# Optimization experiments

Measured on AMD Instinct MI355X. Metric: run time of the kernel, lower is better.

Reference implementation:

```python
import jax, jax.numpy as jnp
import numpy as np

B, L, H, E = 8, 1024, 8, 64  # self-attention: S=L, D=E
SCALE = 1.0 / np.sqrt(E).astype(np.float32)


def setup_inputs() -> dict:
    key = jax.random.key(0)
    ks = jax.random.split(key, 6)
    shp = (B, L, H, E)
    names = ["q_re", "q_im", "k_re", "k_im", "v_re", "v_im"]
    return {n: jax.random.normal(k, shp, dtype=jnp.float32) for n, k in zip(names, ks)}


def reference(q_re, q_im, k_re, k_im, v_re, v_im):
    q = jax.lax.complex(q_re, q_im)  # [B,L,H,E] complex64
    k = jax.lax.complex(k_re, k_im)  # [B,S,H,E] complex64
    # complex QK^T (no conjugate, matching torch einsum semantics)
    scores = jnp.einsum('blhe,bshe->bhls', q, k)      # [B,H,L,S] complex64
    A = jax.nn.softmax(SCALE * jnp.abs(scores), axis=-1)  # [B,H,L,S] real
    # A is promoted to complex with zero imaginary part in the original;
    # multiplying complex V by a real A is equivalent per real/imag part.
    V_re = jnp.einsum('bhls,bshd->blhd', A, v_re)     # [B,L,H,D]
    V_im = jnp.einsum('bhls,bshd->blhd', A, v_im)     # [B,L,H,D]
    return jnp.stack([V_re, V_im], axis=-1)           # [B,L,H,D,2] (re, im)
```

## Files before the change

### kernel.cpp

```cpp
#include <hip/hip_runtime.h>


#define B_ 8
#define L_ 1024
#define H_ 8
#define E_ 64
#define SB 64
#define QB 128
#define NT 16
#define IMG_BYTES 32768
#define WS_NEEDED (64ull * NT * IMG_BYTES)
#define C_EXP 0.18033688011112042f

typedef float  f32x4  __attribute__((ext_vector_type(4)));
typedef float  f32x16 __attribute__((ext_vector_type(16)));
typedef __bf16 bf16x8 __attribute__((ext_vector_type(8)));
typedef unsigned short u16x8 __attribute__((ext_vector_type(8)));
typedef unsigned short u16x4 __attribute__((ext_vector_type(4)));
typedef unsigned int   u32x4 __attribute__((ext_vector_type(4)));

static __device__ __forceinline__ unsigned short f2b(float f) {
    __bf16 h = (__bf16)f;
    return __builtin_bit_cast(unsigned short, h);
}

static __device__ __forceinline__ float fsqrt_(float x) {
    return __builtin_amdgcn_sqrtf(x);
}
static __device__ __forceinline__ float fexp2_(float x) {
    return __builtin_amdgcn_exp2f(x);
}

static __device__ __forceinline__ u16x8 pack8(float4 a, float4 b) {
    u16x8 t;
    t[0]=f2b(a.x); t[1]=f2b(a.y); t[2]=f2b(a.z); t[3]=f2b(a.w);
    t[4]=f2b(b.x); t[5]=f2b(b.y); t[6]=f2b(b.z); t[7]=f2b(b.w);
    return t;
}

static __device__ __forceinline__ f32x16 mfma32(u16x8 a, u16x8 b, f32x16 c) {
    return __builtin_amdgcn_mfma_f32_32x32x16_bf16(
        __builtin_bit_cast(bf16x8, a), __builtin_bit_cast(bf16x8, b), c, 0, 0, 0);
}

static __device__ __forceinline__ unsigned int cvtpk(float lo, float hi) {
    unsigned int r;
    asm("v_cvt_pk_bf16_f32 %0, %1, %2" : "=v"(r) : "v"(lo), "v"(hi));
    return r;
}

static __device__ __forceinline__ void plswap(unsigned int& x, unsigned int& y) {
    asm("v_permlane32_swap_b32 %0, %1" : "+v"(x), "+v"(y));
}

static __device__ __forceinline__ void gload16(const void* g, void* l) {
    __builtin_amdgcn_global_load_lds(
        (const __attribute__((address_space(1))) void*)g,
        (__attribute__((address_space(3))) void*)l,
        16, 0, 0);
}

__global__ __launch_bounds__(256) void ffa_prepack(
    const float* __restrict__ k_re, const float* __restrict__ k_im,
    const float* __restrict__ v_re, const float* __restrict__ v_im,
    char* __restrict__ ws)
{
    const int tid = threadIdx.x;
    const int bh  = blockIdx.x >> 4;
    const int st  = blockIdx.x & 15;
    const int b   = bh >> 3;
    const int h   = bh & 7;
    const int s0  = st * SB;
    char* const img = ws + (size_t)blockIdx.x * IMG_BYTES;

    {
        const int sr = tid >> 2;
        const int sc = (tid & 3) * 16;
        const int kg = ((b * L_ + s0 + sr) * H_ + h) * E_ + sc;
        const float4* pr = (const float4*)(k_re + kg);
        const float4* pi = (const float4*)(k_im + kg);
        float4 r0 = pr[0], r1 = pr[1], r2 = pr[2], r3 = pr[3];
        float4 i0 = pi[0], i1 = pi[1], i2 = pi[2], i3 = pi[3];
        const int krow = sr * 256;
        const int ksw  = (sr & 7) << 4;
        *(u16x8*)(img + ((krow + sc * 2           ) ^ ksw)) = pack8(r0, r1);
        *(u16x8*)(img + ((krow + sc * 2 + 16      ) ^ ksw)) = pack8(r2, r3);
        *(u16x8*)(img + ((krow + 128 + sc * 2     ) ^ ksw)) = pack8(i0, i1);
        *(u16x8*)(img + ((krow + 128 + sc * 2 + 16) ^ ksw)) = pack8(i2, i3);
    }

    {
        const int vtens = tid >> 7;
        const int vd    = ((tid >> 4) & 7) * 8;
        const int vs    = (tid & 15) * 4;
        const float* const vsrc = vtens ? v_im : v_re;
        float vv[4][8];
#pragma unroll
        for (int j = 0; j < 4; ++j) {
            const float4* p = (const float4*)(vsrc + ((b * L_ + s0 + vs + j) * H_ + h) * E_ + vd);
            float4 x = p[0], y = p[1];
            vv[j][0]=x.x; vv[j][1]=x.y; vv[j][2]=x.z; vv[j][3]=x.w;
            vv[j][4]=y.x; vv[j][5]=y.y; vv[j][6]=y.z; vv[j][7]=y.w;
        }
        char* const vimg = img + 16384;
#pragma unroll
        for (int i = 0; i < 8; ++i) {
            const int row = vtens * 64 + vd + i;
            u16x4 t;
            t[0]=f2b(vv[0][i]); t[1]=f2b(vv[1][i]); t[2]=f2b(vv[2][i]); t[3]=f2b(vv[3][i]);
            *(u16x4*)(vimg + ((row * 128 + vs * 2) ^ ((row & 7) << 4))) = t;
        }
    }
}

__global__ __launch_bounds__(256) void ffa_main(
    const float* __restrict__ q_re, const float* __restrict__ q_im,
    const char* __restrict__ ws, float* __restrict__ out)
{
    __shared__ __align__(16) char Buf[2][IMG_BYTES];

    const int tid  = threadIdx.x;
    const int lane = tid & 63;
    const int w    = tid >> 6;
    const int l31  = lane & 31;
    const int h    = lane >> 5;

    const int work = (blockIdx.x & 7) * 64 + (blockIdx.x >> 3);
    const int bh   = work >> 3;
    const int qblk = work & 7;
    const int b    = bh >> 3;
    const int hh   = bh & 7;
    const char* const imgs = ws + (size_t)bh * (NT * IMG_BYTES);

#pragma unroll
    for (int i = 0; i < 8; ++i)
        gload16(imgs + i * 4096 + tid * 16, Buf[0] + i * 4096 + tid * 16);

    u16x8 qre[4], qim[4], qimn[4];
    {
        const int qrow = qblk * QB + w * 32 + l31;
        const int base = ((b * L_ + qrow) * H_ + hh) * E_;
#pragma unroll
        for (int ks = 0; ks < 4; ++ks) {
            const float4* pr = (const float4*)(q_re + base + ks * 16 + h * 8);
            const float4* pi = (const float4*)(q_im + base + ks * 16 + h * 8);
            qre[ks] = pack8(pr[0], pr[1]);
            qim[ks] = pack8(pi[0], pi[1]);
#pragma unroll
            for (int i = 0; i < 8; ++i)
                qimn[ks][i] = (unsigned short)(qim[ks][i] ^ 0x8000u);
        }
    }

    f32x16 oR0 = {}, oR1 = {}, oI0 = {}, oI1 = {};
    float lsum = 0.f;
    const f32x16 z16 = {};
    const int hsw = (h << 4) ^ ((l31 & 7) << 4);

    asm volatile("s_waitcnt vmcnt(0)" ::: "memory");
    __syncthreads();

    for (int st = 0; st < NT; ++st) {
        const int cur = st & 1;
        if (st + 1 < NT) {
            const char* src = imgs + (size_t)(st + 1) * IMG_BYTES;
            char* dst = Buf[cur ^ 1];
#pragma unroll
            for (int i = 0; i < 8; ++i)
                gload16(src + i * 4096 + tid * 16, dst + i * 4096 + tid * 16);
        }
        const char* const kb = Buf[cur];
        const char* const vb = kb + 16384;

        u16x8 pa[4];

#pragma unroll
        for (int kh = 0; kh < 2; ++kh) {
            const char* krow = kb + kh * 8192 + l31 * 256;
            u16x8 kreF[4], kimF[4];
#pragma unroll
            for (int ks = 0; ks < 4; ++ks) {
                kreF[ks] = *(const u16x8*)(krow + ((      ks * 32) ^ hsw));
                kimF[ks] = *(const u16x8*)(krow + ((128 + ks * 32) ^ hsw));
            }
            __builtin_amdgcn_s_setprio(1);
            f32x16 sR = mfma32(kreF[0], qre[0], z16);
            f32x16 sI = mfma32(kimF[0], qre[0], z16);
            sR = mfma32(kimF[0], qimn[0], sR);
            sI = mfma32(kreF[0], qim[0],  sI);
#pragma unroll
            for (int ks = 1; ks < 4; ++ks) {
                sR = mfma32(kreF[ks], qre[ks],  sR);
                sI = mfma32(kimF[ks], qre[ks],  sI);
                sR = mfma32(kimF[ks], qimn[ks], sR);
                sI = mfma32(kreF[ks], qim[ks],  sI);
            }
            __builtin_amdgcn_s_setprio(0);

            float p[16];
#pragma unroll
            for (int r = 0; r < 16; ++r) {
                float re = sR[r], im = sI[r];
                float mag = fsqrt_(fmaf(re, re, im * im));
                p[r] = fexp2_(mag * C_EXP);
            }
            lsum += (((p[0]+p[1])+(p[2]+p[3])) + ((p[4]+p[5])+(p[6]+p[7])))
                  + (((p[8]+p[9])+(p[10]+p[11])) + ((p[12]+p[13])+(p[14]+p[15])));

            unsigned int a0 = cvtpk(p[0],  p[1]),  a1 = cvtpk(p[4],  p[5]);
            unsigned int a2 = cvtpk(p[2],  p[3]),  a3 = cvtpk(p[6],  p[7]);
            unsigned int b0 = cvtpk(p[8],  p[9]),  b1 = cvtpk(p[12], p[13]);
            unsigned int b2 = cvtpk(p[10], p[11]), b3 = cvtpk(p[14], p[15]);
            plswap(a0, a1);
            plswap(a2, a3);
            plswap(b0, b1);
            plswap(b2, b3);
            u32x4 wa = {a0, a2, a1, a3};
            u32x4 wb = {b0, b2, b1, b3};
            pa[2 * kh]     = __builtin_bit_cast(u16x8, wa);
            pa[2 * kh + 1] = __builtin_bit_cast(u16x8, wb);
        }

        {
            const char* vrow = vb + l31 * 128;
            __builtin_amdgcn_s_setprio(1);
#pragma unroll
            for (int ks = 0; ks < 4; ++ks) {
                const int off = (ks * 32) ^ hsw;
                u16x8 vre0 = *(const u16x8*)(vrow +         off);
                u16x8 vre1 = *(const u16x8*)(vrow +  4096 + off);
                u16x8 vim0 = *(const u16x8*)(vrow +  8192 + off);
                u16x8 vim1 = *(const u16x8*)(vrow + 12288 + off);
                oR0 = mfma32(pa[ks], vre0, oR0);
                oR1 = mfma32(pa[ks], vre1, oR1);
                oI0 = mfma32(pa[ks], vim0, oI0);
                oI1 = mfma32(pa[ks], vim1, oI1);
            }
            __builtin_amdgcn_s_setprio(0);
        }

        asm volatile("s_waitcnt vmcnt(0)" ::: "memory");
        __syncthreads();
    }

    lsum += __shfl_xor(lsum, 32);
    const float inv = 1.0f / lsum;
#pragma unroll
    for (int r = 0; r < 16; ++r) {
        const int qs = (r & 3) + 8 * (r >> 2) + 4 * h;
        const float iv = __shfl(inv, qs);
        const int lq = qblk * QB + w * 32 + qs;
        float* op = out + ((b * L_ + lq) * H_ + hh) * (E_ * 2);
        float2 v0 = make_float2(oR0[r] * iv, oI0[r] * iv);
        float2 v1 = make_float2(oR1[r] * iv, oI1[r] * iv);
        *(float2*)(op + l31 * 2)      = v0;
        *(float2*)(op + 64 + l31 * 2) = v1;
    }
}

__global__ __launch_bounds__(256) void ffa_fwd_fb(
    const float* __restrict__ q_re, const float* __restrict__ q_im,
    const float* __restrict__ k_re, const float* __restrict__ k_im,
    const float* __restrict__ v_re, const float* __restrict__ v_im,
    float* __restrict__ out)
{
    __shared__ __align__(16) unsigned short Kt[64 * 128];
    __shared__ __align__(16) unsigned short Vt[128 * 64];
    __shared__ __align__(16) unsigned short Pw[4 * 16 * 64];
    char* const kb = (char*)Kt;
    char* const vb = (char*)Vt;

    const int tid  = threadIdx.x;
    const int lane = tid & 63;
    const int w    = tid >> 6;
    const int lr   = lane & 15;
    const int lg   = lane >> 4;
    const int lg16 = lg * 16;
    const int qblk = blockIdx.x & 15;
    const int bh   = blockIdx.x >> 4;
    const int b    = bh >> 3;
    const int h    = bh & 7;

    u16x8 qre[2], qim[2], qimn[2];
    {
        const int qrow = qblk * 64 + w * 16 + lr;
        const int base = ((b * L_ + qrow) * H_ + h) * E_ + lg * 8;
#pragma unroll
        for (int ks = 0; ks < 2; ++ks) {
            const float4* pr = (const float4*)(q_re + base + ks * 32);
            const float4* pi = (const float4*)(q_im + base + ks * 32);
            qre[ks] = pack8(pr[0], pr[1]);
            qim[ks] = pack8(pi[0], pi[1]);
#pragma unroll
            for (int i = 0; i < 8; ++i)
                qimn[ks][i] = (unsigned short)(qim[ks][i] ^ 0x8000u);
        }
    }

    float lsum[4];
    f32x4 Ore[4], Oim[4];
    const f32x4 zero = {0.f, 0.f, 0.f, 0.f};
#pragma unroll
    for (int r = 0; r < 4; ++r) lsum[r] = 0.f;
#pragma unroll
    for (int dt = 0; dt < 4; ++dt) { Ore[dt] = zero; Oim[dt] = zero; }

    const int sr = tid >> 2;
    const int sc = (tid & 3) * 16;
    const int vtens = tid >> 7;
    const int vd    = ((tid >> 4) & 7) * 8;
    const int vs    = (tid & 15) * 4;
    const float* const vsrc = vtens ? v_im : v_re;

    for (int st = 0; st < L_ / SB; ++st) {
        const int s0 = st * SB;
        {
            const int kg = ((b * L_ + s0 + sr) * H_ + h) * E_ + sc;
            const float4* pr = (const float4*)(k_re + kg);
            const float4* pi = (const float4*)(k_im + kg);
            float4 r0 = pr[0], r1 = pr[1], r2 = pr[2], r3 = pr[3];
            float4 i0 = pi[0], i1 = pi[1], i2 = pi[2], i3 = pi[3];
            const int krow = sr * 256;
            const int ksw  = (sr & 7) << 4;
            *(u16x8*)(kb + ((krow + sc * 2           ) ^ ksw)) = pack8(r0, r1);
            *(u16x8*)(kb + ((krow + sc * 2 + 16      ) ^ ksw)) = pack8(r2, r3);
            *(u16x8*)(kb + ((krow + 128 + sc * 2     ) ^ ksw)) = pack8(i0, i1);
            *(u16x8*)(kb + ((krow + 128 + sc * 2 + 16) ^ ksw)) = pack8(i2, i3);
        }
        {
            float vv[4][8];
#pragma unroll
            for (int j = 0; j < 4; ++j) {
                const float4* p = (const float4*)(vsrc + ((b * L_ + s0 + vs + j) * H_ + h) * E_ + vd);
                float4 x = p[0], y = p[1];
                vv[j][0]=x.x; vv[j][1]=x.y; vv[j][2]=x.z; vv[j][3]=x.w;
                vv[j][4]=y.x; vv[j][5]=y.y; vv[j][6]=y.z; vv[j][7]=y.w;
            }
#pragma unroll
            for (int i = 0; i < 8; ++i) {
                const int row = vtens * 64 + vd + i;
                u16x4 t;
                t[0]=f2b(vv[0][i]); t[1]=f2b(vv[1][i]); t[2]=f2b(vv[2][i]); t[3]=f2b(vv[3][i]);
                *(u16x4*)(vb + ((row * 128 + vs * 2) ^ ((row & 7) << 4))) = t;
            }
        }
        __syncthreads();

        f32x4 aR[4], aI[4];
#pragma unroll
        for (int t = 0; t < 4; ++t) { aR[t] = zero; aI[t] = zero; }
#pragma unroll
        for (int t = 0; t < 4; ++t) {
            const int key = t * 16 + lr;
            const char* kr = kb + key * 256;
            const int sw = (key & 7) << 4;
            u16x8 br0 = *(const u16x8*)(kr + (( lg16      ) ^ sw));
            u16x8 br1 = *(const u16x8*)(kr + (( 64 + lg16 ) ^ sw));
            u16x8 bi0 = *(const u16x8*)(kr + ((128 + lg16 ) ^ sw));
            u16x8 bi1 = *(const u16x8*)(kr + ((192 + lg16 ) ^ sw));
            aR[t] = __builtin_amdgcn_mfma_f32_16x16x32_bf16(__builtin_bit_cast(bf16x8,qre[0]),  __builtin_bit_cast(bf16x8,br0), aR[t],0,0,0);
            aR[t] = __builtin_amdgcn_mfma_f32_16x16x32_bf16(__builtin_bit_cast(bf16x8,qre[1]),  __builtin_bit_cast(bf16x8,br1), aR[t],0,0,0);
            aR[t] = __builtin_amdgcn_mfma_f32_16x16x32_bf16(__builtin_bit_cast(bf16x8,qimn[0]), __builtin_bit_cast(bf16x8,bi0), aR[t],0,0,0);
            aR[t] = __builtin_amdgcn_mfma_f32_16x16x32_bf16(__builtin_bit_cast(bf16x8,qimn[1]), __builtin_bit_cast(bf16x8,bi1), aR[t],0,0,0);
            aI[t] = __builtin_amdgcn_mfma_f32_16x16x32_bf16(__builtin_bit_cast(bf16x8,qre[0]),  __builtin_bit_cast(bf16x8,bi0), aI[t],0,0,0);
            aI[t] = __builtin_amdgcn_mfma_f32_16x16x32_bf16(__builtin_bit_cast(bf16x8,qre[1]),  __builtin_bit_cast(bf16x8,bi1), aI[t],0,0,0);
            aI[t] = __builtin_amdgcn_mfma_f32_16x16x32_bf16(__builtin_bit_cast(bf16x8,qim[0]),  __builtin_bit_cast(bf16x8,br0), aI[t],0,0,0);
            aI[t] = __builtin_amdgcn_mfma_f32_16x16x32_bf16(__builtin_bit_cast(bf16x8,qim[1]),  __builtin_bit_cast(bf16x8,br1), aI[t],0,0,0);
        }

        float p_[4][4];
#pragma unroll
        for (int t = 0; t < 4; ++t)
#pragma unroll
            for (int r = 0; r < 4; ++r) {
                float re = aR[t][r], im = aI[t][r];
                p_[t][r] = fexp2_(fsqrt_(fmaf(re, re, im * im)) * C_EXP);
            }
#pragma unroll
        for (int r = 0; r < 4; ++r)
            lsum[r] += (p_[0][r] + p_[1][r]) + (p_[2][r] + p_[3][r]);

        char* const pb = (char*)Pw + w * 2048;
#pragma unroll
        for (int t = 0; t < 4; ++t)
#pragma unroll
            for (int r = 0; r < 4; ++r) {
                const int prow = lg * 4 + r;
                *(unsigned short*)(pb + ((prow * 128 + (t * 16 + lr) * 2) ^ ((prow & 7) << 4)))
                    = f2b(p_[t][r]);
            }
        asm volatile("s_waitcnt lgkmcnt(0)" ::: "memory");
        __builtin_amdgcn_sched_barrier(0);
        const int psw = (lr & 7) << 4;
        u16x8 pf0 = *(const u16x8*)(pb + ((lr * 128 + lg16     ) ^ psw));
        u16x8 pf1 = *(const u16x8*)(pb + ((lr * 128 + 64 + lg16) ^ psw));

#pragma unroll
        for (int dt = 0; dt < 4; ++dt) {
            const int dr = dt * 16 + lr;
            const int swr = (dr & 7) << 4;
            const char* vrre = vb + dr * 128;
            const char* vrim = vb + (64 + dr) * 128;
            u16x8 vr0 = *(const u16x8*)(vrre + (( lg16     ) ^ swr));
            u16x8 vr1 = *(const u16x8*)(vrre + (( 64 + lg16) ^ swr));
            u16x8 vi0 = *(const u16x8*)(vrim + (( lg16     ) ^ swr));
            u16x8 vi1 = *(const u16x8*)(vrim + (( 64 + lg16) ^ swr));
            Ore[dt] = __builtin_amdgcn_mfma_f32_16x16x32_bf16(__builtin_bit_cast(bf16x8,pf0), __builtin_bit_cast(bf16x8,vr0), Ore[dt],0,0,0);
            Ore[dt] = __builtin_amdgcn_mfma_f32_16x16x32_bf16(__builtin_bit_cast(bf16x8,pf1), __builtin_bit_cast(bf16x8,vr1), Ore[dt],0,0,0);
            Oim[dt] = __builtin_amdgcn_mfma_f32_16x16x32_bf16(__builtin_bit_cast(bf16x8,pf0), __builtin_bit_cast(bf16x8,vi0), Oim[dt],0,0,0);
            Oim[dt] = __builtin_amdgcn_mfma_f32_16x16x32_bf16(__builtin_bit_cast(bf16x8,pf1), __builtin_bit_cast(bf16x8,vi1), Oim[dt],0,0,0);
        }
        __syncthreads();
    }

#pragma unroll
    for (int r = 0; r < 4; ++r) {
        float s = lsum[r];
        s += __shfl_xor(s, 1);
        s += __shfl_xor(s, 2);
        s += __shfl_xor(s, 4);
        s += __shfl_xor(s, 8);
        const float inv = 1.0f / s;
        const int lq = qblk * 64 + w * 16 + lg * 4 + r;
        const int obase = (((b * L_ + lq) * H_ + h) * E_) * 2;
#pragma unroll
        for (int dt = 0; dt < 4; ++dt) {
            const int d = dt * 16 + lr;
            float2 val = make_float2(Ore[dt][r] * inv, Oim[dt][r] * inv);
            *(float2*)(out + obase + d * 2) = val;
        }
    }
}

extern "C" void kernel_launch(void* const* d_in, const int* in_sizes, int n_in,
                              void* d_out, int out_size, void* d_ws, size_t ws_size,
                              hipStream_t stream) {
    const float* q_re = (const float*)d_in[0];
    const float* q_im = (const float*)d_in[1];
    const float* k_re = (const float*)d_in[2];
    const float* k_im = (const float*)d_in[3];
    const float* v_re = (const float*)d_in[4];
    const float* v_im = (const float*)d_in[5];
    float* out = (float*)d_out;

    if (ws_size >= WS_NEEDED) {
        char* ws = (char*)d_ws;
        hipLaunchKernelGGL(ffa_prepack, dim3(B_ * H_ * NT), dim3(256), 0, stream,
                           k_re, k_im, v_re, v_im, ws);
        hipLaunchKernelGGL(ffa_main, dim3(B_ * H_ * (L_ / QB)), dim3(256), 0, stream,
                           q_re, q_im, (const char*)ws, out);
    } else {
        hipLaunchKernelGGL(ffa_fwd_fb, dim3(B_ * H_ * (L_ / 64)), dim3(256), 0, stream,
                           q_re, q_im, k_re, k_im, v_re, v_im, out);
    }
}
```

Baseline: 95.42 us.

## Prepack K/V into per-lane MFMA fragment order and load directly from global

The prepack kernel now writes K and V tiles already arranged as per-lane MFMA operand fragments. The main kernel reads them straight from global/L2 into registers, which removes the LDS double buffer, the swizzled LDS reads and the per-tile barriers. The QK chain is split into two independent accumulators for more MFMA ILP, the negated q_im is recomputed on the fly to save registers, and launch bounds request 2 blocks per CU. The cost is that every wave fetches the K/V image separately through the cache instead of sharing one LDS copy, and V prepack becomes strided scalar gathers.

Result: faster. 90.48 us (-5.2%).

```diff
diff --git a/kernel.cpp b/kernel.cpp
--- a/kernel.cpp
+++ b/kernel.cpp
@@ -53,11 +53,10 @@
     asm("v_permlane32_swap_b32 %0, %1" : "+v"(x), "+v"(y));
 }
 
-static __device__ __forceinline__ void gload16(const void* g, void* l) {
-    __builtin_amdgcn_global_load_lds(
-        (const __attribute__((address_space(1))) void*)g,
-        (__attribute__((address_space(3))) void*)l,
-        16, 0, 0);
+static __device__ __forceinline__ u16x8 negbf8(u16x8 a) {
+    u32x4 u = __builtin_bit_cast(u32x4, a);
+    u[0] ^= 0x80008000u; u[1] ^= 0x80008000u; u[2] ^= 0x80008000u; u[3] ^= 0x80008000u;
+    return __builtin_bit_cast(u16x8, u);
 }
 
 __global__ __launch_bounds__(256) void ffa_prepack(
@@ -73,52 +72,45 @@
     const int s0  = st * SB;
     char* const img = ws + (size_t)blockIdx.x * IMG_BYTES;
 
-    {
-        const int sr = tid >> 2;
-        const int sc = (tid & 3) * 16;
-        const int kg = ((b * L_ + s0 + sr) * H_ + h) * E_ + sc;
-        const float4* pr = (const float4*)(k_re + kg);
-        const float4* pi = (const float4*)(k_im + kg);
-        float4 r0 = pr[0], r1 = pr[1], r2 = pr[2], r3 = pr[3];
-        float4 i0 = pi[0], i1 = pi[1], i2 = pi[2], i3 = pi[3];
-        const int krow = sr * 256;
-        const int ksw  = (sr & 7) << 4;
-        *(u16x8*)(img + ((krow + sc * 2           ) ^ ksw)) = pack8(r0, r1);
-        *(u16x8*)(img + ((krow + sc * 2 + 16      ) ^ ksw)) = pack8(r2, r3);
-        *(u16x8*)(img + ((krow + 128 + sc * 2     ) ^ ksw)) = pack8(i0, i1);
-        *(u16x8*)(img + ((krow + 128 + sc * 2 + 16) ^ ksw)) = pack8(i2, i3);
-    }
-
-    {
-        const int vtens = tid >> 7;
-        const int vd    = ((tid >> 4) & 7) * 8;
-        const int vs    = (tid & 15) * 4;
-        const float* const vsrc = vtens ? v_im : v_re;
-        float vv[4][8];
-#pragma unroll
-        for (int j = 0; j < 4; ++j) {
-            const float4* p = (const float4*)(vsrc + ((b * L_ + s0 + vs + j) * H_ + h) * E_ + vd);
-            float4 x = p[0], y = p[1];
-            vv[j][0]=x.x; vv[j][1]=x.y; vv[j][2]=x.z; vv[j][3]=x.w;
-            vv[j][4]=y.x; vv[j][5]=y.y; vv[j][6]=y.z; vv[j][7]=y.w;
-        }
-        char* const vimg = img + 16384;
-#pragma unroll
-        for (int i = 0; i < 8; ++i) {
-            const int row = vtens * 64 + vd + i;
-            u16x4 t;
-            t[0]=f2b(vv[0][i]); t[1]=f2b(vv[1][i]); t[2]=f2b(vv[2][i]); t[3]=f2b(vv[3][i]);
-            *(u16x4*)(vimg + ((row * 128 + vs * 2) ^ ((row & 7) << 4))) = t;
-        }
-    }
-}
-
-__global__ __launch_bounds__(256) void ffa_main(
+    const int l   = tid & 63;
+    const int fg  = tid >> 6;
+    const int l31 = l & 31;
+    const int lh  = l >> 5;
+
+#pragma unroll
+    for (int ff = 0; ff < 8; ++ff) {
+        const int f = fg * 8 + ff;
+        u16x8 val;
+        if (f < 16) {
+            const int kh = f >> 3, ks = (f >> 1) & 3, c = f & 1;
+            const float* src = (c ? k_im : k_re)
+                + ((size_t)((b * L_ + s0 + kh * 32 + l31) * H_ + h)) * E_ + ks * 16 + lh * 8;
+            const float4* p = (const float4*)src;
+            val = pack8(p[0], p[1]);
+        } else {
+            const int g = f - 16, ks = g >> 2, j = g & 3;
+            const float* src = (j >= 2) ? v_im : v_re;
+            const int d = (j & 1) * 32 + l31;
+            const int sb = s0 + ks * 16 + lh * 8;
+            float4 t0, t1;
+            t0.x = src[((size_t)((b * L_ + sb + 0) * H_ + h)) * E_ + d];
+            t0.y = src[((size_t)((b * L_ + sb + 1) * H_ + h)) * E_ + d];
+            t0.z = src[((size_t)((b * L_ + sb + 2) * H_ + h)) * E_ + d];
+            t0.w = src[((size_t)((b * L_ + sb + 3) * H_ + h)) * E_ + d];
+            t1.x = src[((size_t)((b * L_ + sb + 4) * H_ + h)) * E_ + d];
+            t1.y = src[((size_t)((b * L_ + sb + 5) * H_ + h)) * E_ + d];
+            t1.z = src[((size_t)((b * L_ + sb + 6) * H_ + h)) * E_ + d];
+            t1.w = src[((size_t)((b * L_ + sb + 7) * H_ + h)) * E_ + d];
+            val = pack8(t0, t1);
+        }
+        *(u16x8*)(img + f * 1024 + l * 16) = val;
+    }
+}
+
+__global__ __launch_bounds__(256, 2) void ffa_main(
     const float* __restrict__ q_re, const float* __restrict__ q_im,
     const char* __restrict__ ws, float* __restrict__ out)
 {
-    __shared__ __align__(16) char Buf[2][IMG_BYTES];
-
     const int tid  = threadIdx.x;
     const int lane = tid & 63;
     const int w    = tid >> 6;
@@ -130,13 +122,9 @@
     const int qblk = work & 7;
     const int b    = bh >> 3;
     const int hh   = bh & 7;
-    const char* const imgs = ws + (size_t)bh * (NT * IMG_BYTES);
-
-#pragma unroll
-    for (int i = 0; i < 8; ++i)
-        gload16(imgs + i * 4096 + tid * 16, Buf[0] + i * 4096 + tid * 16);
-
-    u16x8 qre[4], qim[4], qimn[4];
+    const char* const imgs = ws + (size_t)bh * (NT * IMG_BYTES) + lane * 16;
+
+    u16x8 qre[4], qim[4];
     {
         const int qrow = qblk * QB + w * 32 + l31;
         const int base = ((b * L_ + qrow) * H_ + hh) * E_;
@@ -146,61 +134,64 @@
             const float4* pi = (const float4*)(q_im + base + ks * 16 + h * 8);
             qre[ks] = pack8(pr[0], pr[1]);
             qim[ks] = pack8(pi[0], pi[1]);
-#pragma unroll
-            for (int i = 0; i < 8; ++i)
-                qimn[ks][i] = (unsigned short)(qim[ks][i] ^ 0x8000u);
         }
     }
 
     f32x16 oR0 = {}, oR1 = {}, oI0 = {}, oI1 = {};
     float lsum = 0.f;
     const f32x16 z16 = {};
-    const int hsw = (h << 4) ^ ((l31 & 7) << 4);
-
-    asm volatile("s_waitcnt vmcnt(0)" ::: "memory");
-    __syncthreads();
 
     for (int st = 0; st < NT; ++st) {
-        const int cur = st & 1;
-        if (st + 1 < NT) {
-            const char* src = imgs + (size_t)(st + 1) * IMG_BYTES;
-            char* dst = Buf[cur ^ 1];
-#pragma unroll
-            for (int i = 0; i < 8; ++i)
-                gload16(src + i * 4096 + tid * 16, dst + i * 4096 + tid * 16);
-        }
-        const char* const kb = Buf[cur];
-        const char* const vb = kb + 16384;
+        const char* const tb = imgs + st * IMG_BYTES;
+
+        u16x8 kf[16];
+#pragma unroll
+        for (int f = 0; f < 16; ++f)
+            kf[f] = *(const u16x8*)(tb + f * 1024);
 
         u16x8 pa[4];
+        u16x8 vf[16];
 
 #pragma unroll
         for (int kh = 0; kh < 2; ++kh) {
-            const char* krow = kb + kh * 8192 + l31 * 256;
-            u16x8 kreF[4], kimF[4];
-#pragma unroll
-            for (int ks = 0; ks < 4; ++ks) {
-                kreF[ks] = *(const u16x8*)(krow + ((      ks * 32) ^ hsw));
-                kimF[ks] = *(const u16x8*)(krow + ((128 + ks * 32) ^ hsw));
-            }
+            const u16x8* K = kf + kh * 8;
+            u16x8 qn0 = negbf8(qim[0]), qn1 = negbf8(qim[1]);
+            u16x8 qn2 = negbf8(qim[2]), qn3 = negbf8(qim[3]);
+
             __builtin_amdgcn_s_setprio(1);
-            f32x16 sR = mfma32(kreF[0], qre[0], z16);
-            f32x16 sI = mfma32(kimF[0], qre[0], z16);
-            sR = mfma32(kimF[0], qimn[0], sR);
-            sI = mfma32(kreF[0], qim[0],  sI);
-#pragma unroll
-            for (int ks = 1; ks < 4; ++ks) {
-                sR = mfma32(kreF[ks], qre[ks],  sR);
-                sI = mfma32(kimF[ks], qre[ks],  sI);
-                sR = mfma32(kimF[ks], qimn[ks], sR);
-                sI = mfma32(kreF[ks], qim[ks],  sI);
-            }
+            f32x16 sR0 = mfma32(K[0], qre[0], z16);
+            f32x16 sI0 = mfma32(K[1], qre[0], z16);
+            f32x16 sR1 = mfma32(K[4], qre[2], z16);
+            f32x16 sI1 = mfma32(K[5], qre[2], z16);
+            sR0 = mfma32(K[1], qn0,    sR0);
+            sI0 = mfma32(K[0], qim[0], sI0);
+            sR1 = mfma32(K[5], qn2,    sR1);
+            sI1 = mfma32(K[4], qim[2], sI1);
+            sR0 = mfma32(K[2], qre[1], sR0);
+            sI0 = mfma32(K[3], qre[1], sI0);
+            sR1 = mfma32(K[6], qre[3], sR1);
+            sI1 = mfma32(K[7], qre[3], sI1);
+            sR0 = mfma32(K[3], qn1,    sR0);
+            sI0 = mfma32(K[2], qim[1], sI0);
+            sR1 = mfma32(K[7], qn3,    sR1);
+            sI1 = mfma32(K[6], qim[3], sI1);
             __builtin_amdgcn_s_setprio(0);
 
+            if (kh == 0) {
+#pragma unroll
+                for (int g = 0; g < 8; ++g)
+                    vf[g] = *(const u16x8*)(tb + (16 + g) * 1024);
+            } else {
+#pragma unroll
+                for (int g = 8; g < 16; ++g)
+                    vf[g] = *(const u16x8*)(tb + (16 + g) * 1024);
+            }
+
             float p[16];
 #pragma unroll
             for (int r = 0; r < 16; ++r) {
-                float re = sR[r], im = sI[r];
+                float re = sR0[r] + sR1[r];
+                float im = sI0[r] + sI1[r];
                 float mag = fsqrt_(fmaf(re, re, im * im));
                 p[r] = fexp2_(mag * C_EXP);
             }
@@ -221,26 +212,15 @@
             pa[2 * kh + 1] = __builtin_bit_cast(u16x8, wb);
         }
 
-        {
-            const char* vrow = vb + l31 * 128;
-            __builtin_amdgcn_s_setprio(1);
-#pragma unroll
-            for (int ks = 0; ks < 4; ++ks) {
-                const int off = (ks * 32) ^ hsw;
-                u16x8 vre0 = *(const u16x8*)(vrow +         off);
-                u16x8 vre1 = *(const u16x8*)(vrow +  4096 + off);
-                u16x8 vim0 = *(const u16x8*)(vrow +  8192 + off);
-                u16x8 vim1 = *(const u16x8*)(vrow + 12288 + off);
-                oR0 = mfma32(pa[ks], vre0, oR0);
-                oR1 = mfma32(pa[ks], vre1, oR1);
-                oI0 = mfma32(pa[ks], vim0, oI0);
-                oI1 = mfma32(pa[ks], vim1, oI1);
-            }
-            __builtin_amdgcn_s_setprio(0);
-        }
-
-        asm volatile("s_waitcnt vmcnt(0)" ::: "memory");
-        __syncthreads();
+        __builtin_amdgcn_s_setprio(1);
+#pragma unroll
+        for (int ks = 0; ks < 4; ++ks) {
+            oR0 = mfma32(pa[ks], vf[ks * 4 + 0], oR0);
+            oR1 = mfma32(pa[ks], vf[ks * 4 + 1], oR1);
+            oI0 = mfma32(pa[ks], vf[ks * 4 + 2], oI0);
+            oI1 = mfma32(pa[ks], vf[ks * 4 + 3], oI1);
+        }
+        __builtin_amdgcn_s_setprio(0);
     }
 
     lsum += __shfl_xor(lsum, 32);
```
